# Kernel optimization log

Hardware: AMD Instinct MI355X
Metric: run time of the kernel (lower is better)

## Reference

```python
import jax, jax.numpy as jnp
import numpy as np

B, N, E, H = 2, 50000, 400000, 128


def _lin_init(k, fan_in, fan_out):
    s = 1.0 / np.sqrt(fan_in)
    kw, kb = jax.random.split(k)
    W = jax.random.uniform(kw, (fan_in, fan_out), jnp.float32, -s, s)
    b = jax.random.uniform(kb, (fan_out,), jnp.float32, -s, s)
    return W, b


def setup_inputs() -> dict:
    key = jax.random.key(0)
    ks = jax.random.split(key, 7)
    x = jax.random.normal(ks[0], (B, N, H), jnp.float32)
    edge_index = jax.random.randint(ks[1], (2, E), 0, N, jnp.int64)
    edge_attr = jax.random.normal(ks[2], (B, E, H), jnp.float32)
    We1, be1 = _lin_init(ks[3], 3 * H, H)
    We2, be2 = _lin_init(ks[4], H, H)
    Wn1, bn1 = _lin_init(ks[5], 2 * H, H)
    Wn2, bn2 = _lin_init(ks[6], H, H)
    return dict(x=x, edge_index=edge_index, edge_attr=edge_attr,
                We1=We1, be1=be1, We2=We2, be2=be2,
                Wn1=Wn1, bn1=bn1, Wn2=Wn2, bn2=bn2)


def reference(x, edge_index, edge_attr, We1, be1, We2, be2, Wn1, bn1, Wn2, bn2):
    src = edge_index[0]
    dest = edge_index[1]
    # edge model: MLP(concat(src_feat, dest_feat, edge_attr))  [B,E,3H] -> [B,E,H]
    m = jnp.concatenate([x[:, src], x[:, dest], edge_attr], axis=-1)
    e = jax.nn.relu(m @ We1 + be1) @ We2 + be2
    # node model: scatter-sum messages to dest nodes, then MLP(concat(x, agg))
    agg = jax.vmap(lambda eb: jax.ops.segment_sum(eb, dest, num_segments=x.shape[1]))(e)
    h = jnp.concatenate([x, agg], axis=-1)  # [B,N,2H]
    x_out = jax.nn.relu(h @ Wn1 + bn1) @ Wn2 + bn2
    return x_out, e
```

## Files before the change

kernel.cpp:

```cpp
#include <hip/hip_runtime.h>
#include <hip/hip_bf16.h>

#define Hd 128
#define Nn 50000
#define Ee 400000
#define Bb 2
#define NROWS 100000

typedef __attribute__((ext_vector_type(8))) short bf16x8;
typedef __attribute__((ext_vector_type(4))) short bf16x4;
typedef __attribute__((ext_vector_type(4))) float f32x4;

static __device__ __forceinline__ short f2bf(float f) {
    __hip_bfloat16 h = __float2bfloat16(f);
    return *reinterpret_cast<short*>(&h);
}
static __device__ __forceinline__ float bf2f(short s) {
    union { unsigned u; float f; } v; v.u = ((unsigned)(unsigned short)s) << 16;
    return v.f;
}
static __device__ __forceinline__ bf16x8 cvt8(float4 a, float4 b) {
    bf16x8 r;
    r[0] = f2bf(a.x); r[1] = f2bf(a.y); r[2] = f2bf(a.z); r[3] = f2bf(a.w);
    r[4] = f2bf(b.x); r[5] = f2bf(b.y); r[6] = f2bf(b.z); r[7] = f2bf(b.w);
    return r;
}
static __device__ __forceinline__ unsigned pk2(float a, float b) {
    return (unsigned)(unsigned short)f2bf(a) | ((unsigned)(unsigned short)f2bf(b) << 16);
}

__global__ void prep_weights(const float* __restrict__ We1, const float* __restrict__ We2,
                             const float* __restrict__ Wn1, const float* __restrict__ Wn2,
                             short* __restrict__ wbuf) {
    int gid = blockIdx.x * 256 + threadIdx.x;
    if (gid < 32768) {
        int c = gid >> 7, k = gid & 127;
        float v = (c < 128) ? We1[k * 128 + c] : We1[(k + 128) * 128 + (c - 128)];
        wbuf[gid] = f2bf(v); return;
    }
    int g = gid - 32768;
    if (g < 16384) { int c = g >> 7, k = g & 127; wbuf[gid] = f2bf(We1[(k + 256) * 128 + c]); return; }
    g -= 16384;
    if (g < 16384) { int c = g >> 7, k = g & 127; wbuf[gid] = f2bf(We2[k * 128 + c]); return; }
    g -= 16384;
    if (g < 32768) { int c = g >> 8, k = g & 255; wbuf[gid] = f2bf(Wn1[k * 128 + c]); return; }
    g -= 32768;
    if (g < 16384) { int c = g >> 7, k = g & 127; wbuf[gid] = f2bf(Wn2[k * 128 + c]); }
}

__global__ void hist_kernel(const int* __restrict__ ei, int* __restrict__ cnt) {
    int t = blockIdx.x * 256 + threadIdx.x;
    if (t < Ee) atomicAdd(&cnt[ei[Ee + t]], 1);
}
__global__ void scan1(const int* __restrict__ cnt, int* __restrict__ cur, int* __restrict__ part) {
    __shared__ int s[256];
    int i = blockIdx.x * 256 + threadIdx.x;
    int v = (i < Nn) ? cnt[i] : 0;
    s[threadIdx.x] = v; __syncthreads();
    #pragma unroll
    for (int off = 1; off < 256; off <<= 1) {
        int u = (threadIdx.x >= off) ? s[threadIdx.x - off] : 0;
        __syncthreads(); s[threadIdx.x] += u; __syncthreads();
    }
    if (i < Nn) cur[i] = s[threadIdx.x] - v;
    if (threadIdx.x == 255) part[blockIdx.x] = s[255];
}
__global__ void scan2(int* __restrict__ part) {
    if (threadIdx.x == 0 && blockIdx.x == 0) {
        int run = 0;
        for (int i = 0; i < 196; i++) { int t = part[i]; part[i] = run; run += t; }
    }
}
__global__ void scan3(int* __restrict__ cur, const int* __restrict__ part, int* __restrict__ rp) {
    int i = blockIdx.x * 256 + threadIdx.x;
    if (i < Nn) { int v = cur[i] + part[blockIdx.x]; cur[i] = v; rp[i] = v; }
    if (i == 0 && blockIdx.x == 0) rp[Nn] = Ee;
}
__global__ void scatter_k(const int* __restrict__ ei, int* __restrict__ cur, int* __restrict__ elist) {
    int t = blockIdx.x * 256 + threadIdx.x;
    if (t < Ee) { int d = ei[Ee + t]; int pos = atomicAdd(&cur[d], 1); elist[pos] = t; }
}

__global__ __launch_bounds__(256) void node_pre(
    const float* __restrict__ x, const short* __restrict__ WabT,
    short* __restrict__ xa, short* __restrict__ xb)
{
    __shared__ __align__(16) short X[32 * 128];

    const int nbase = blockIdx.x * 32;
    const int t = threadIdx.x;
    const int wv = t >> 6, lane = t & 63;
    const int row16 = lane & 15, kg = lane >> 4;

    {
        int g = t >> 3, q = t & 7;
        const float* src = x + ((size_t)(nbase + g)) * Hd + q * 16;
        float4 a0 = ((const float4*)src)[0], a1 = ((const float4*)src)[1];
        float4 a2 = ((const float4*)src)[2], a3 = ((const float4*)src)[3];
        ((bf16x8*)X)[g * 16 + ((q * 2) ^ (g & 7))]     = cvt8(a0, a1);
        ((bf16x8*)X)[g * 16 + ((q * 2 + 1) ^ (g & 7))] = cvt8(a2, a3);
    }

    bf16x8 wf[4][4];
    #pragma unroll
    for (int nt = 0; nt < 4; nt++) {
        int n = wv * 64 + nt * 16 + row16;
        #pragma unroll
        for (int kt = 0; kt < 4; kt++)
            wf[kt][nt] = *(const bf16x8*)(WabT + n * 128 + kt * 32 + kg * 8);
    }
    __syncthreads();

    f32x4 acc[2][4];
    #pragma unroll
    for (int mt = 0; mt < 2; mt++)
        #pragma unroll
        for (int nt = 0; nt < 4; nt++) acc[mt][nt] = (f32x4){0.f,0.f,0.f,0.f};

    #pragma unroll
    for (int mt = 0; mt < 2; mt++) {
        int row = mt * 16 + row16;
        #pragma unroll
        for (int kt = 0; kt < 4; kt++) {
            bf16x8 xf = ((const bf16x8*)X)[row * 16 + ((kt * 4 + kg) ^ (row & 7))];
            #pragma unroll
            for (int nt = 0; nt < 4; nt++)
                acc[mt][nt] = __builtin_amdgcn_mfma_f32_16x16x32_bf16(wf[kt][nt], xf, acc[mt][nt], 0, 0, 0);
        }
    }

    #pragma unroll
    for (int mt = 0; mt < 2; mt++) {
        size_t node = nbase + mt * 16 + row16;
        #pragma unroll
        for (int nt = 0; nt < 4; nt++) {
            int ch = wv * 64 + nt * 16 + kg * 4;
            uint2 pk = { pk2(acc[mt][nt][0], acc[mt][nt][1]), pk2(acc[mt][nt][2], acc[mt][nt][3]) };
            short* dst = (ch < 128) ? (xa + node * Hd + ch) : (xb + node * Hd + (ch - 128));
            *(uint2*)dst = pk;
        }
    }
}

__global__ __launch_bounds__(512, 4) void edge_mlp(
    const float* __restrict__ ea, const int* __restrict__ ei,
    const short* __restrict__ xa, const short* __restrict__ xb,
    const short* __restrict__ W1cT, const float* __restrict__ be1,
    const short* __restrict__ W2T, const float* __restrict__ be2,
    float* __restrict__ e_out)
{
    __shared__ __align__(16) short Aea[64 * 128];
    __shared__ __align__(16) short A2[64 * 128];

    const int bid = blockIdx.x;
    const int b = bid / (Ee / 64);
    const int ebase = (bid % (Ee / 64)) * 64;
    const int t = threadIdx.x;
    const int wv = t >> 6, lane = t & 63;
    const int row16 = lane & 15, kg = lane >> 4;
    const int n0 = wv * 16 + kg * 4;

    {
        int row = t >> 3, q = t & 7;
        const float* src = ea + ((size_t)b * Ee + ebase + row) * Hd + q * 16;
        float4 a0 = ((const float4*)src)[0], a1 = ((const float4*)src)[1];
        float4 a2 = ((const float4*)src)[2], a3 = ((const float4*)src)[3];
        ((bf16x8*)Aea)[row * 16 + ((q * 2) ^ (row & 7))]     = cvt8(a0, a1);
        ((bf16x8*)Aea)[row * 16 + ((q * 2 + 1) ^ (row & 7))] = cvt8(a2, a3);
    }

    bf16x8 w1[4];
    {
        const short* wp = W1cT + (wv * 16 + row16) * 128 + kg * 8;
        #pragma unroll
        for (int kt = 0; kt < 4; kt++) w1[kt] = *(const bf16x8*)(wp + kt * 32);
    }
    int sn[4], dn[4];
    #pragma unroll
    for (int mt = 0; mt < 4; mt++) {
        int eidx = ebase + mt * 16 + row16;
        sn[mt] = ei[eidx]; dn[mt] = ei[Ee + eidx];
    }
    __syncthreads();

    f32x4 acc[4];
    #pragma unroll
    for (int mt = 0; mt < 4; mt++) acc[mt] = (f32x4){0.f,0.f,0.f,0.f};
    #pragma unroll
    for (int kt = 0; kt < 4; kt++) {
        #pragma unroll
        for (int mt = 0; mt < 4; mt++) {
            int row = mt * 16 + row16;
            bf16x8 af = ((const bf16x8*)Aea)[row * 16 + ((kt * 4 + kg) ^ (row & 7))];
            acc[mt] = __builtin_amdgcn_mfma_f32_16x16x32_bf16(w1[kt], af, acc[mt], 0, 0, 0);
        }
    }

    bf16x4 av[4], bv[4];
    #pragma unroll
    for (int mt = 0; mt < 4; mt++) {
        av[mt] = *(const bf16x4*)(xa + ((size_t)b * Nn + sn[mt]) * Hd + n0);
        bv[mt] = *(const bf16x4*)(xb + ((size_t)b * Nn + dn[mt]) * Hd + n0);
    }
    float4 b1v = *(const float4*)(be1 + n0);

    bf16x8 w2[4];
    {
        const short* wp = W2T + (wv * 16 + row16) * 128 + kg * 8;
        #pragma unroll
        for (int kt = 0; kt < 4; kt++) w2[kt] = *(const bf16x8*)(wp + kt * 32);
    }

    #pragma unroll
    for (int mt = 0; mt < 4; mt++) {
        int row = mt * 16 + row16;
        float v[4];
        #pragma unroll
        for (int r = 0; r < 4; r++) {
            float u = acc[mt][r] + b1v[r] + bf2f(av[mt][r]) + bf2f(bv[mt][r]);
            v[r] = u > 0.f ? u : 0.f;
        }
        int G = (n0 >> 3) ^ (row & 7);
        *(uint2*)((char*)A2 + row * 256 + G * 16 + (n0 & 7) * 2) = (uint2){ pk2(v[0], v[1]), pk2(v[2], v[3]) };
    }
    __syncthreads();

    f32x4 acc2[4];
    #pragma unroll
    for (int mt = 0; mt < 4; mt++) acc2[mt] = (f32x4){0.f,0.f,0.f,0.f};
    #pragma unroll
    for (int kt = 0; kt < 4; kt++) {
        #pragma unroll
        for (int mt = 0; mt < 4; mt++) {
            int row = mt * 16 + row16;
            bf16x8 hf = *(const bf16x8*)((const char*)A2 + row * 256 + (((kt * 4 + kg) ^ (row & 7)) * 16));
            acc2[mt] = __builtin_amdgcn_mfma_f32_16x16x32_bf16(w2[kt], hf, acc2[mt], 0, 0, 0);
        }
    }
    float4 b2v = *(const float4*)(be2 + n0);
    float* eo = e_out + ((size_t)b * Ee + ebase) * Hd;
    #pragma unroll
    for (int mt = 0; mt < 4; mt++) {
        float4 ov;
        ov.x = acc2[mt][0] + b2v.x;
        ov.y = acc2[mt][1] + b2v.y;
        ov.z = acc2[mt][2] + b2v.z;
        ov.w = acc2[mt][3] + b2v.w;
        *(float4*)(eo + (size_t)(mt * 16 + row16) * Hd + n0) = ov;
    }
}

__global__ __launch_bounds__(512, 4) void node_mlp(
    const float* __restrict__ x, const float* __restrict__ e_out,
    const int* __restrict__ rp, const int* __restrict__ elist,
    const short* __restrict__ Wn1T, const float* __restrict__ bn1,
    const short* __restrict__ Wn2T, const float* __restrict__ bn2,
    float* __restrict__ xout)
{
    __shared__ __align__(16) short A[32 * 256];
    __shared__ __align__(16) short A2[32 * 128];

    const int tilesPerB = (Nn + 31) / 32;
    const int bid = blockIdx.x;
    const int b = bid / tilesPerB;
    const int nbase = (bid % tilesPerB) * 32;
    const int t = threadIdx.x;
    const int wv = t >> 6, lane = t & 63;
    const int row16 = lane & 15, kg = lane >> 4;
    const int n0 = wv * 16 + kg * 4;

    {
        int g = t >> 4, q2 = t & 15;
        int n = nbase + g;
        float4 xv0 = {0,0,0,0}, xv1 = xv0;
        float4 s0 = {0,0,0,0}, s1 = s0;
        if (n < Nn) {
            const float* xr = x + ((size_t)b * Nn + n) * Hd + q2 * 8;
            xv0 = ((const float4*)xr)[0]; xv1 = ((const float4*)xr)[1];
            int jb = rp[n], je = rp[n + 1];
            const float* eb = e_out + (size_t)b * Ee * Hd + q2 * 8;
            int j = jb;
            for (; j + 4 <= je; j += 4) {
                int e0 = elist[j], e1 = elist[j+1], e2 = elist[j+2], e3 = elist[j+3];
                const float* p0 = eb + (size_t)e0 * Hd;
                const float* p1 = eb + (size_t)e1 * Hd;
                const float* p2 = eb + (size_t)e2 * Hd;
                const float* p3 = eb + (size_t)e3 * Hd;
                float4 u0 = ((const float4*)p0)[0], u1 = ((const float4*)p0)[1];
                float4 u2 = ((const float4*)p1)[0], u3 = ((const float4*)p1)[1];
                float4 u4 = ((const float4*)p2)[0], u5 = ((const float4*)p2)[1];
                float4 u6 = ((const float4*)p3)[0], u7 = ((const float4*)p3)[1];
                s0.x += (u0.x + u2.x) + (u4.x + u6.x);
                s0.y += (u0.y + u2.y) + (u4.y + u6.y);
                s0.z += (u0.z + u2.z) + (u4.z + u6.z);
                s0.w += (u0.w + u2.w) + (u4.w + u6.w);
                s1.x += (u1.x + u3.x) + (u5.x + u7.x);
                s1.y += (u1.y + u3.y) + (u5.y + u7.y);
                s1.z += (u1.z + u3.z) + (u5.z + u7.z);
                s1.w += (u1.w + u3.w) + (u5.w + u7.w);
            }
            for (; j < je; j++) {
                const float* p0 = eb + (size_t)elist[j] * Hd;
                float4 u0 = ((const float4*)p0)[0], u1 = ((const float4*)p0)[1];
                s0.x += u0.x; s0.y += u0.y; s0.z += u0.z; s0.w += u0.w;
                s1.x += u1.x; s1.y += u1.y; s1.z += u1.z; s1.w += u1.w;
            }
        }
        ((bf16x8*)A)[g * 32 + (q2 ^ (g & 7))]        = cvt8(xv0, xv1);
        ((bf16x8*)A)[g * 32 + ((16 + q2) ^ (g & 7))] = cvt8(s0, s1);
    }

    bf16x8 w1[8];
    {
        const short* wp = Wn1T + (wv * 16 + row16) * 256 + kg * 8;
        #pragma unroll
        for (int kt = 0; kt < 8; kt++) w1[kt] = *(const bf16x8*)(wp + kt * 32);
    }
    __syncthreads();

    f32x4 acc[2];
    acc[0] = (f32x4){0.f,0.f,0.f,0.f}; acc[1] = (f32x4){0.f,0.f,0.f,0.f};
    #pragma unroll
    for (int kt = 0; kt < 8; kt++) {
        #pragma unroll
        for (int mt = 0; mt < 2; mt++) {
            int row = mt * 16 + row16;
            bf16x8 af = ((const bf16x8*)A)[row * 32 + ((kt * 4 + kg) ^ (row & 7))];
            acc[mt] = __builtin_amdgcn_mfma_f32_16x16x32_bf16(w1[kt], af, acc[mt], 0, 0, 0);
        }
    }

    float4 b1v = *(const float4*)(bn1 + n0);
    bf16x8 w2[4];
    {
        const short* wp = Wn2T + (wv * 16 + row16) * 128 + kg * 8;
        #pragma unroll
        for (int kt = 0; kt < 4; kt++) w2[kt] = *(const bf16x8*)(wp + kt * 32);
    }

    #pragma unroll
    for (int mt = 0; mt < 2; mt++) {
        int row = mt * 16 + row16;
        float v[4];
        #pragma unroll
        for (int r = 0; r < 4; r++) {
            float u = acc[mt][r] + b1v[r];
            v[r] = u > 0.f ? u : 0.f;
        }
        int G = (n0 >> 3) ^ (row & 7);
        *(uint2*)((char*)A2 + row * 256 + G * 16 + (n0 & 7) * 2) = (uint2){ pk2(v[0], v[1]), pk2(v[2], v[3]) };
    }
    __syncthreads();

    f32x4 acc2[2];
    acc2[0] = (f32x4){0.f,0.f,0.f,0.f}; acc2[1] = (f32x4){0.f,0.f,0.f,0.f};
    #pragma unroll
    for (int kt = 0; kt < 4; kt++) {
        #pragma unroll
        for (int mt = 0; mt < 2; mt++) {
            int row = mt * 16 + row16;
            bf16x8 hf = *(const bf16x8*)((const char*)A2 + row * 256 + (((kt * 4 + kg) ^ (row & 7)) * 16));
            acc2[mt] = __builtin_amdgcn_mfma_f32_16x16x32_bf16(w2[kt], hf, acc2[mt], 0, 0, 0);
        }
    }
    float4 b2v = *(const float4*)(bn2 + n0);
    #pragma unroll
    for (int mt = 0; mt < 2; mt++) {
        int node = nbase + mt * 16 + row16;
        if (node < Nn) {
            float4 ov;
            ov.x = acc2[mt][0] + b2v.x;
            ov.y = acc2[mt][1] + b2v.y;
            ov.z = acc2[mt][2] + b2v.z;
            ov.w = acc2[mt][3] + b2v.w;
            *(float4*)(xout + ((size_t)b * Nn + node) * Hd + n0) = ov;
        }
    }
}

extern "C" void kernel_launch(void* const* d_in, const int* in_sizes, int n_in,
                              void* d_out, int out_size, void* d_ws, size_t ws_size,
                              hipStream_t stream) {
    const float* x   = (const float*)d_in[0];
    const int*   ei  = (const int*)d_in[1];
    const float* ea  = (const float*)d_in[2];
    const float* We1 = (const float*)d_in[3];
    const float* be1 = (const float*)d_in[4];
    const float* We2 = (const float*)d_in[5];
    const float* be2 = (const float*)d_in[6];
    const float* Wn1 = (const float*)d_in[7];
    const float* bn1 = (const float*)d_in[8];
    const float* Wn2 = (const float*)d_in[9];
    const float* bn2 = (const float*)d_in[10];

    float* xout  = (float*)d_out;
    float* e_out = xout + (size_t)Bb * Nn * Hd;

    short* wbuf  = (short*)d_ws;
    short* xa    = wbuf + 114688;
    short* xb    = xa + (size_t)NROWS * Hd;
    int*   cnt   = (int*)(xb + (size_t)NROWS * Hd);
    int*   cur   = cnt + Nn;
    int*   rp    = cur + Nn;
    int*   part  = rp + Nn + 1;
    int*   elist = part + 256;

    hipMemsetAsync(cnt, 0, Nn * sizeof(int), stream);
    prep_weights<<<448, 256, 0, stream>>>(We1, We2, Wn1, Wn2, wbuf);
    hist_kernel<<<(Ee + 255) / 256, 256, 0, stream>>>(ei, cnt);
    scan1<<<196, 256, 0, stream>>>(cnt, cur, part);
    scan2<<<1, 64, 0, stream>>>(part);
    scan3<<<196, 256, 0, stream>>>(cur, part, rp);
    scatter_k<<<(Ee + 255) / 256, 256, 0, stream>>>(ei, cur, elist);

    node_pre<<<NROWS / 32, 256, 0, stream>>>(x, wbuf, xa, xb);

    edge_mlp<<<Bb * (Ee / 64), 512, 0, stream>>>(
        ea, ei, xa, xb, wbuf + 32768, be1, wbuf + 49152, be2, e_out);

    node_mlp<<<Bb * ((Nn + 31) / 32), 512, 0, stream>>>(
        x, e_out, rp, elist, wbuf + 65536, bn1, wbuf + 98304, bn2, xout);
}
```

Measured before the change: 505.3 us.

## Make edge MLP persistent over tile chunks with software-pipelined prefetch

Each edge_mlp block now processes a chunk of six 64-edge tiles instead of one, loading the weight fragments once per block. The edge_attr rows, edge indices and gathered node features for the next tile are prefetched into registers while the current tile's MFMAs run, with the LDS staging buffer double-buffered. This aims to hide global-memory latency and amortize weight loads, at the cost of higher register pressure (possibly lower occupancy) and fewer blocks in the grid.

```diff
diff --git a/kernel.cpp b/kernel.cpp
--- a/kernel.cpp
+++ b/kernel.cpp
@@ -6,6 +6,8 @@
 #define Ee 400000
 #define Bb 2
 #define NROWS 100000
+#define NT 12500
+#define CHUNK 6
 
 typedef __attribute__((ext_vector_type(8))) short bf16x8;
 typedef __attribute__((ext_vector_type(4))) short bf16x4;
@@ -27,6 +29,11 @@
 }
 static __device__ __forceinline__ unsigned pk2(float a, float b) {
     return (unsigned)(unsigned short)f2bf(a) | ((unsigned)(unsigned short)f2bf(b) << 16);
+}
+static __device__ __forceinline__ void lds_barrier() {
+    asm volatile("s_waitcnt lgkmcnt(0)" ::: "memory");
+    __builtin_amdgcn_s_barrier();
+    asm volatile("" ::: "memory");
 }
 
 __global__ void prep_weights(const float* __restrict__ We1, const float* __restrict__ We2,
@@ -149,104 +156,157 @@
     const short* __restrict__ W2T, const float* __restrict__ be2,
     float* __restrict__ e_out)
 {
-    __shared__ __align__(16) short Aea[64 * 128];
+    __shared__ __align__(16) short Aea[2][64 * 128];
     __shared__ __align__(16) short A2[64 * 128];
 
-    const int bid = blockIdx.x;
-    const int b = bid / (Ee / 64);
-    const int ebase = (bid % (Ee / 64)) * 64;
     const int t = threadIdx.x;
     const int wv = t >> 6, lane = t & 63;
     const int row16 = lane & 15, kg = lane >> 4;
     const int n0 = wv * 16 + kg * 4;
-
+    const int srow = t >> 3, sq = t & 7;
+
+    bf16x8 w1[4], w2[4];
     {
-        int row = t >> 3, q = t & 7;
-        const float* src = ea + ((size_t)b * Ee + ebase + row) * Hd + q * 16;
-        float4 a0 = ((const float4*)src)[0], a1 = ((const float4*)src)[1];
-        float4 a2 = ((const float4*)src)[2], a3 = ((const float4*)src)[3];
-        ((bf16x8*)Aea)[row * 16 + ((q * 2) ^ (row & 7))]     = cvt8(a0, a1);
-        ((bf16x8*)Aea)[row * 16 + ((q * 2 + 1) ^ (row & 7))] = cvt8(a2, a3);
-    }
-
-    bf16x8 w1[4];
-    {
-        const short* wp = W1cT + (wv * 16 + row16) * 128 + kg * 8;
-        #pragma unroll
-        for (int kt = 0; kt < 4; kt++) w1[kt] = *(const bf16x8*)(wp + kt * 32);
-    }
-    int sn[4], dn[4];
-    #pragma unroll
-    for (int mt = 0; mt < 4; mt++) {
-        int eidx = ebase + mt * 16 + row16;
-        sn[mt] = ei[eidx]; dn[mt] = ei[Ee + eidx];
-    }
-    __syncthreads();
-
-    f32x4 acc[4];
-    #pragma unroll
-    for (int mt = 0; mt < 4; mt++) acc[mt] = (f32x4){0.f,0.f,0.f,0.f};
-    #pragma unroll
-    for (int kt = 0; kt < 4; kt++) {
+        const short* wp1 = W1cT + (wv * 16 + row16) * 128 + kg * 8;
+        const short* wp2 = W2T  + (wv * 16 + row16) * 128 + kg * 8;
+        #pragma unroll
+        for (int kt = 0; kt < 4; kt++) {
+            w1[kt] = *(const bf16x8*)(wp1 + kt * 32);
+            w2[kt] = *(const bf16x8*)(wp2 + kt * 32);
+        }
+    }
+    #pragma unroll
+    for (int kt = 0; kt < 4; kt++) { asm volatile("" : "+v"(w1[kt]), "+v"(w2[kt])); }
+    const float4 b1v = *(const float4*)(be1 + n0);
+    const float4 b2v = *(const float4*)(be2 + n0);
+
+    int tile = blockIdx.x * CHUNK;
+
+    float4 er0, er1, er2, er3;
+    bf16x4 av[4], bv[4];
+    if (tile < NT) {
+        int b = tile / (Ee / 64);
+        int ebase = (tile % (Ee / 64)) * 64;
+        const float* src = ea + ((size_t)b * Ee + ebase + srow) * Hd + sq * 16;
+        er0 = ((const float4*)src)[0]; er1 = ((const float4*)src)[1];
+        er2 = ((const float4*)src)[2]; er3 = ((const float4*)src)[3];
+        int sn[4], dn[4];
         #pragma unroll
         for (int mt = 0; mt < 4; mt++) {
-            int row = mt * 16 + row16;
-            bf16x8 af = ((const bf16x8*)Aea)[row * 16 + ((kt * 4 + kg) ^ (row & 7))];
-            acc[mt] = __builtin_amdgcn_mfma_f32_16x16x32_bf16(w1[kt], af, acc[mt], 0, 0, 0);
-        }
-    }
-
-    bf16x4 av[4], bv[4];
-    #pragma unroll
-    for (int mt = 0; mt < 4; mt++) {
-        av[mt] = *(const bf16x4*)(xa + ((size_t)b * Nn + sn[mt]) * Hd + n0);
-        bv[mt] = *(const bf16x4*)(xb + ((size_t)b * Nn + dn[mt]) * Hd + n0);
-    }
-    float4 b1v = *(const float4*)(be1 + n0);
-
-    bf16x8 w2[4];
-    {
-        const short* wp = W2T + (wv * 16 + row16) * 128 + kg * 8;
-        #pragma unroll
-        for (int kt = 0; kt < 4; kt++) w2[kt] = *(const bf16x8*)(wp + kt * 32);
-    }
-
-    #pragma unroll
-    for (int mt = 0; mt < 4; mt++) {
-        int row = mt * 16 + row16;
-        float v[4];
-        #pragma unroll
-        for (int r = 0; r < 4; r++) {
-            float u = acc[mt][r] + b1v[r] + bf2f(av[mt][r]) + bf2f(bv[mt][r]);
-            v[r] = u > 0.f ? u : 0.f;
-        }
-        int G = (n0 >> 3) ^ (row & 7);
-        *(uint2*)((char*)A2 + row * 256 + G * 16 + (n0 & 7) * 2) = (uint2){ pk2(v[0], v[1]), pk2(v[2], v[3]) };
-    }
-    __syncthreads();
-
-    f32x4 acc2[4];
-    #pragma unroll
-    for (int mt = 0; mt < 4; mt++) acc2[mt] = (f32x4){0.f,0.f,0.f,0.f};
-    #pragma unroll
-    for (int kt = 0; kt < 4; kt++) {
+            int eidx = ebase + mt * 16 + row16;
+            sn[mt] = ei[eidx]; dn[mt] = ei[Ee + eidx];
+        }
+        const short* xab = xa + (size_t)b * Nn * Hd;
+        const short* xbb = xb + (size_t)b * Nn * Hd;
         #pragma unroll
         for (int mt = 0; mt < 4; mt++) {
-            int row = mt * 16 + row16;
-            bf16x8 hf = *(const bf16x8*)((const char*)A2 + row * 256 + (((kt * 4 + kg) ^ (row & 7)) * 16));
-            acc2[mt] = __builtin_amdgcn_mfma_f32_16x16x32_bf16(w2[kt], hf, acc2[mt], 0, 0, 0);
-        }
-    }
-    float4 b2v = *(const float4*)(be2 + n0);
-    float* eo = e_out + ((size_t)b * Ee + ebase) * Hd;
-    #pragma unroll
-    for (int mt = 0; mt < 4; mt++) {
-        float4 ov;
-        ov.x = acc2[mt][0] + b2v.x;
-        ov.y = acc2[mt][1] + b2v.y;
-        ov.z = acc2[mt][2] + b2v.z;
-        ov.w = acc2[mt][3] + b2v.w;
-        *(float4*)(eo + (size_t)(mt * 16 + row16) * Hd + n0) = ov;
+            av[mt] = *(const bf16x4*)(xab + (size_t)sn[mt] * Hd + n0);
+            bv[mt] = *(const bf16x4*)(xbb + (size_t)dn[mt] * Hd + n0);
+        }
+    }
+
+    int cur = 0;
+    for (int it = 0; it < CHUNK; ++it) {
+        const bool v = (tile < NT);
+        const int b = tile / (Ee / 64);
+        const size_t ebase = (size_t)(tile % (Ee / 64)) * 64;
+
+        if (v) {
+            ((bf16x8*)Aea[cur])[srow * 16 + ((sq * 2)     ^ (srow & 7))] = cvt8(er0, er1);
+            ((bf16x8*)Aea[cur])[srow * 16 + ((sq * 2 + 1) ^ (srow & 7))] = cvt8(er2, er3);
+        }
+        lds_barrier();
+
+        const int ntile = tile + 1;
+        const bool nv = (it + 1 < CHUNK) && (ntile < NT);
+        float4 ner0, ner1, ner2, ner3;
+        int nsn[4], ndn[4];
+        int nb = 0; int nebase = 0;
+        if (nv) {
+            nb = ntile / (Ee / 64);
+            nebase = (ntile % (Ee / 64)) * 64;
+            const float* src = ea + ((size_t)nb * Ee + nebase + srow) * Hd + sq * 16;
+            ner0 = ((const float4*)src)[0]; ner1 = ((const float4*)src)[1];
+            ner2 = ((const float4*)src)[2]; ner3 = ((const float4*)src)[3];
+            #pragma unroll
+            for (int mt = 0; mt < 4; mt++) {
+                int eidx = nebase + mt * 16 + row16;
+                nsn[mt] = ei[eidx]; ndn[mt] = ei[Ee + eidx];
+            }
+        }
+
+        f32x4 acc[4];
+        #pragma unroll
+        for (int mt = 0; mt < 4; mt++) acc[mt] = (f32x4){0.f,0.f,0.f,0.f};
+        if (v) {
+            #pragma unroll
+            for (int kt = 0; kt < 4; kt++) {
+                #pragma unroll
+                for (int mt = 0; mt < 4; mt++) {
+                    int row = mt * 16 + row16;
+                    bf16x8 af = ((const bf16x8*)Aea[cur])[row * 16 + ((kt * 4 + kg) ^ (row & 7))];
+                    acc[mt] = __builtin_amdgcn_mfma_f32_16x16x32_bf16(w1[kt], af, acc[mt], 0, 0, 0);
+                }
+            }
+        }
+
+        bf16x4 nav[4], nbv[4];
+        if (nv) {
+            const short* xab = xa + (size_t)nb * Nn * Hd;
+            const short* xbb = xb + (size_t)nb * Nn * Hd;
+            #pragma unroll
+            for (int mt = 0; mt < 4; mt++) {
+                nav[mt] = *(const bf16x4*)(xab + (size_t)nsn[mt] * Hd + n0);
+                nbv[mt] = *(const bf16x4*)(xbb + (size_t)ndn[mt] * Hd + n0);
+            }
+        }
+
+        if (v) {
+            #pragma unroll
+            for (int mt = 0; mt < 4; mt++) {
+                int row = mt * 16 + row16;
+                float vv[4];
+                #pragma unroll
+                for (int r = 0; r < 4; r++) {
+                    float u = acc[mt][r] + b1v[r] + bf2f(av[mt][r]) + bf2f(bv[mt][r]);
+                    vv[r] = u > 0.f ? u : 0.f;
+                }
+                int G = (n0 >> 3) ^ (row & 7);
+                *(uint2*)((char*)A2 + row * 256 + G * 16 + (n0 & 7) * 2) =
+                    (uint2){ pk2(vv[0], vv[1]), pk2(vv[2], vv[3]) };
+            }
+        }
+        lds_barrier();
+
+        if (v) {
+            f32x4 acc2[4];
+            #pragma unroll
+            for (int mt = 0; mt < 4; mt++) acc2[mt] = (f32x4){0.f,0.f,0.f,0.f};
+            #pragma unroll
+            for (int kt = 0; kt < 4; kt++) {
+                #pragma unroll
+                for (int mt = 0; mt < 4; mt++) {
+                    int row = mt * 16 + row16;
+                    bf16x8 hf = *(const bf16x8*)((const char*)A2 + row * 256 + (((kt * 4 + kg) ^ (row & 7)) * 16));
+                    acc2[mt] = __builtin_amdgcn_mfma_f32_16x16x32_bf16(w2[kt], hf, acc2[mt], 0, 0, 0);
+                }
+            }
+            float* eo = e_out + ((size_t)b * Ee + ebase) * Hd;
+            #pragma unroll
+            for (int mt = 0; mt < 4; mt++) {
+                float4 ov;
+                ov.x = acc2[mt][0] + b2v.x;
+                ov.y = acc2[mt][1] + b2v.y;
+                ov.z = acc2[mt][2] + b2v.z;
+                ov.w = acc2[mt][3] + b2v.w;
+                *(float4*)(eo + (size_t)(mt * 16 + row16) * Hd + n0) = ov;
+            }
+        }
+
+        er0 = ner0; er1 = ner1; er2 = ner2; er3 = ner3;
+        #pragma unroll
+        for (int mt = 0; mt < 4; mt++) { av[mt] = nav[mt]; bv[mt] = nbv[mt]; }
+        cur ^= 1; tile = ntile;
     }
 }
 
@@ -415,7 +475,7 @@
 
     node_pre<<<NROWS / 32, 256, 0, stream>>>(x, wbuf, xa, xb);
 
-    edge_mlp<<<Bb * (Ee / 64), 512, 0, stream>>>(
+    edge_mlp<<<(NT + CHUNK - 1) / CHUNK, 512, 0, stream>>>(
         ea, ei, xa, xb, wbuf + 32768, be1, wbuf + 49152, be2, e_out);
 
     node_mlp<<<Bb * ((Nn + 31) / 32), 512, 0, stream>>>(
```

Measured after the change: 580.3 us. 14.8% more time.

## Pre-gather summed src/dest node projections into a contiguous edge buffer

Applied to the files above, without the earlier changes.

Adds an xs_pre kernel that gathers the per-edge src and dest projected node features, adds them, and writes a contiguous bf16 [B,E,H] buffer. The edge MLP kernel then reads this buffer with coalesced loads instead of doing random gathers inside the MFMA kernel. It also replaces the barriers with an explicit lgkmcnt wait plus s_barrier. The cost is an extra kernel launch and about 200 MB of extra write and read traffic. The path is only taken when the workspace is large enough, otherwise the old gather kernel runs.

```diff
diff --git a/kernel.cpp b/kernel.cpp
--- a/kernel.cpp
+++ b/kernel.cpp
@@ -6,6 +6,8 @@
 #define Ee 400000
 #define Bb 2
 #define NROWS 100000
+#define TPB 6250
+#define NT 12500
 
 typedef __attribute__((ext_vector_type(8))) short bf16x8;
 typedef __attribute__((ext_vector_type(4))) short bf16x4;
@@ -27,6 +29,10 @@
 }
 static __device__ __forceinline__ unsigned pk2(float a, float b) {
     return (unsigned)(unsigned short)f2bf(a) | ((unsigned)(unsigned short)f2bf(b) << 16);
+}
+static __device__ __forceinline__ void lds_barrier() {
+    asm volatile("s_waitcnt lgkmcnt(0)" ::: "memory");
+    __builtin_amdgcn_s_barrier();
 }
 
 __global__ void prep_weights(const float* __restrict__ We1, const float* __restrict__ We2,
@@ -142,7 +148,129 @@
     }
 }
 
-__global__ __launch_bounds__(512, 4) void edge_mlp(
+__global__ __launch_bounds__(256) void xs_pre(
+    const int* __restrict__ ei, const short* __restrict__ xa,
+    const short* __restrict__ xb, short* __restrict__ xs)
+{
+    int gid = blockIdx.x * 256 + threadIdx.x;
+    int c = gid & 3;
+    int e = (gid >> 2) % Ee;
+    int b = gid / (Ee * 4);
+    int s = ei[e], d = ei[Ee + e];
+    const short* xar = xa + ((size_t)b * Nn + s) * Hd + c * 32;
+    const short* xbr = xb + ((size_t)b * Nn + d) * Hd + c * 32;
+    short* dst = xs + ((size_t)b * Ee + e) * Hd + c * 32;
+    #pragma unroll
+    for (int g = 0; g < 4; g++) {
+        bf16x8 a8 = ((const bf16x8*)xar)[g];
+        bf16x8 b8 = ((const bf16x8*)xbr)[g];
+        bf16x8 o;
+        #pragma unroll
+        for (int j = 0; j < 8; j++) o[j] = f2bf(bf2f(a8[j]) + bf2f(b8[j]));
+        ((bf16x8*)dst)[g] = o;
+    }
+}
+
+__global__ __launch_bounds__(512) void edge_mlp_xs(
+    const float* __restrict__ ea, const short* __restrict__ xs,
+    const short* __restrict__ W1cT, const float* __restrict__ be1,
+    const short* __restrict__ W2T, const float* __restrict__ be2,
+    float* __restrict__ e_out)
+{
+    __shared__ __align__(16) short Aea[64 * 128];
+    __shared__ __align__(16) short A2[64 * 128];
+
+    const int bid = blockIdx.x;
+    const int b = bid / TPB;
+    const size_t ebase = (size_t)(bid % TPB) * 64;
+    const int t = threadIdx.x;
+    const int wv = t >> 6, lane = t & 63;
+    const int row16 = lane & 15, kg = lane >> 4;
+    const int n0 = wv * 16 + kg * 4;
+
+    {
+        int row = t >> 3, q = t & 7;
+        const float* src = ea + ((size_t)b * Ee + ebase + row) * Hd + q * 16;
+        float4 a0 = ((const float4*)src)[0], a1 = ((const float4*)src)[1];
+        float4 a2 = ((const float4*)src)[2], a3 = ((const float4*)src)[3];
+        ((bf16x8*)Aea)[row * 16 + ((q * 2) ^ (row & 7))]     = cvt8(a0, a1);
+        ((bf16x8*)Aea)[row * 16 + ((q * 2 + 1) ^ (row & 7))] = cvt8(a2, a3);
+    }
+
+    bf16x8 w1[4], w2[4];
+    {
+        const short* wp1 = W1cT + (wv * 16 + row16) * 128 + kg * 8;
+        const short* wp2 = W2T  + (wv * 16 + row16) * 128 + kg * 8;
+        #pragma unroll
+        for (int kt = 0; kt < 4; kt++) {
+            w1[kt] = *(const bf16x8*)(wp1 + kt * 32);
+            w2[kt] = *(const bf16x8*)(wp2 + kt * 32);
+        }
+    }
+    bf16x4 xv[4];
+    {
+        const short* xsb = xs + ((size_t)b * Ee + ebase) * Hd + n0;
+        #pragma unroll
+        for (int mt = 0; mt < 4; mt++)
+            xv[mt] = *(const bf16x4*)(xsb + (size_t)(mt * 16 + row16) * Hd);
+    }
+    const float4 b1v = *(const float4*)(be1 + n0);
+    const float4 b2v = *(const float4*)(be2 + n0);
+    lds_barrier();
+
+    f32x4 acc[4];
+    #pragma unroll
+    for (int mt = 0; mt < 4; mt++) acc[mt] = (f32x4){0.f,0.f,0.f,0.f};
+    #pragma unroll
+    for (int kt = 0; kt < 4; kt++) {
+        #pragma unroll
+        for (int mt = 0; mt < 4; mt++) {
+            int row = mt * 16 + row16;
+            bf16x8 af = ((const bf16x8*)Aea)[row * 16 + ((kt * 4 + kg) ^ (row & 7))];
+            acc[mt] = __builtin_amdgcn_mfma_f32_16x16x32_bf16(w1[kt], af, acc[mt], 0, 0, 0);
+        }
+    }
+
+    #pragma unroll
+    for (int mt = 0; mt < 4; mt++) {
+        int row = mt * 16 + row16;
+        float vv[4];
+        #pragma unroll
+        for (int r = 0; r < 4; r++) {
+            float u = acc[mt][r] + b1v[r] + bf2f(xv[mt][r]);
+            vv[r] = u > 0.f ? u : 0.f;
+        }
+        int G = (n0 >> 3) ^ (row & 7);
+        *(uint2*)((char*)A2 + row * 256 + G * 16 + (n0 & 7) * 2) =
+            (uint2){ pk2(vv[0], vv[1]), pk2(vv[2], vv[3]) };
+    }
+    lds_barrier();
+
+    f32x4 acc2[4];
+    #pragma unroll
+    for (int mt = 0; mt < 4; mt++) acc2[mt] = (f32x4){0.f,0.f,0.f,0.f};
+    #pragma unroll
+    for (int kt = 0; kt < 4; kt++) {
+        #pragma unroll
+        for (int mt = 0; mt < 4; mt++) {
+            int row = mt * 16 + row16;
+            bf16x8 hf = *(const bf16x8*)((const char*)A2 + row * 256 + (((kt * 4 + kg) ^ (row & 7)) * 16));
+            acc2[mt] = __builtin_amdgcn_mfma_f32_16x16x32_bf16(w2[kt], hf, acc2[mt], 0, 0, 0);
+        }
+    }
+    float* eo = e_out + ((size_t)b * Ee + ebase) * Hd;
+    #pragma unroll
+    for (int mt = 0; mt < 4; mt++) {
+        float4 ov;
+        ov.x = acc2[mt][0] + b2v.x;
+        ov.y = acc2[mt][1] + b2v.y;
+        ov.z = acc2[mt][2] + b2v.z;
+        ov.w = acc2[mt][3] + b2v.w;
+        *(float4*)(eo + (size_t)(mt * 16 + row16) * Hd + n0) = ov;
+    }
+}
+
+__global__ __launch_bounds__(512, 4) void edge_mlp_gather(
     const float* __restrict__ ea, const int* __restrict__ ei,
     const short* __restrict__ xa, const short* __restrict__ xb,
     const short* __restrict__ W1cT, const float* __restrict__ be1,
@@ -153,8 +281,8 @@
     __shared__ __align__(16) short A2[64 * 128];
 
     const int bid = blockIdx.x;
-    const int b = bid / (Ee / 64);
-    const int ebase = (bid % (Ee / 64)) * 64;
+    const int b = bid / TPB;
+    const size_t ebase = (size_t)(bid % TPB) * 64;
     const int t = threadIdx.x;
     const int wv = t >> 6, lane = t & 63;
     const int row16 = lane & 15, kg = lane >> 4;
@@ -168,7 +296,6 @@
         ((bf16x8*)Aea)[row * 16 + ((q * 2) ^ (row & 7))]     = cvt8(a0, a1);
         ((bf16x8*)Aea)[row * 16 + ((q * 2 + 1) ^ (row & 7))] = cvt8(a2, a3);
     }
-
     bf16x8 w1[4];
     {
         const short* wp = W1cT + (wv * 16 + row16) * 128 + kg * 8;
@@ -178,7 +305,7 @@
     int sn[4], dn[4];
     #pragma unroll
     for (int mt = 0; mt < 4; mt++) {
-        int eidx = ebase + mt * 16 + row16;
+        int eidx = (int)ebase + mt * 16 + row16;
         sn[mt] = ei[eidx]; dn[mt] = ei[Ee + eidx];
     }
     __syncthreads();
@@ -195,7 +322,6 @@
             acc[mt] = __builtin_amdgcn_mfma_f32_16x16x32_bf16(w1[kt], af, acc[mt], 0, 0, 0);
         }
     }
-
     bf16x4 av[4], bv[4];
     #pragma unroll
     for (int mt = 0; mt < 4; mt++) {
@@ -203,14 +329,12 @@
         bv[mt] = *(const bf16x4*)(xb + ((size_t)b * Nn + dn[mt]) * Hd + n0);
     }
     float4 b1v = *(const float4*)(be1 + n0);
-
     bf16x8 w2[4];
     {
         const short* wp = W2T + (wv * 16 + row16) * 128 + kg * 8;
         #pragma unroll
         for (int kt = 0; kt < 4; kt++) w2[kt] = *(const bf16x8*)(wp + kt * 32);
     }
-
     #pragma unroll
     for (int mt = 0; mt < 4; mt++) {
         int row = mt * 16 + row16;
@@ -396,14 +520,18 @@
     float* xout  = (float*)d_out;
     float* e_out = xout + (size_t)Bb * Nn * Hd;
 
-    short* wbuf  = (short*)d_ws;
-    short* xa    = wbuf + 114688;
+    char* w = (char*)d_ws;
+    short* wbuf  = (short*)w;
+    short* xa    = (short*)(w + 229376);
     short* xb    = xa + (size_t)NROWS * Hd;
     int*   cnt   = (int*)(xb + (size_t)NROWS * Hd);
     int*   cur   = cnt + Nn;
     int*   rp    = cur + Nn;
     int*   part  = rp + Nn + 1;
     int*   elist = part + 256;
+    short* xs    = (short*)(elist + Ee);
+    size_t need  = (size_t)((char*)(xs + (size_t)Bb * Ee * Hd) - w);
+    bool use_xs  = (ws_size >= need);
 
     hipMemsetAsync(cnt, 0, Nn * sizeof(int), stream);
     prep_weights<<<448, 256, 0, stream>>>(We1, We2, Wn1, Wn2, wbuf);
@@ -415,8 +543,14 @@
 
     node_pre<<<NROWS / 32, 256, 0, stream>>>(x, wbuf, xa, xb);
 
-    edge_mlp<<<Bb * (Ee / 64), 512, 0, stream>>>(
-        ea, ei, xa, xb, wbuf + 32768, be1, wbuf + 49152, be2, e_out);
+    if (use_xs) {
+        xs_pre<<<(Bb * Ee * 4) / 256, 256, 0, stream>>>(ei, xa, xb, xs);
+        edge_mlp_xs<<<NT, 512, 0, stream>>>(
+            ea, xs, wbuf + 32768, be1, wbuf + 49152, be2, e_out);
+    } else {
+        edge_mlp_gather<<<NT, 512, 0, stream>>>(
+            ea, ei, xa, xb, wbuf + 32768, be1, wbuf + 49152, be2, e_out);
+    }
 
     node_mlp<<<Bb * ((Nn + 31) / 32), 512, 0, stream>>>(
         x, e_out, rp, elist, wbuf + 65536, bn1, wbuf + 98304, bn2, xout);
```

Measured after the change: 563.8 us. +11.6%, slower.

## Fuse scatter-sum into edge MLP via dest-sorted edge tiles and atomics

Applied to the files above, without the earlier changes.

The edge MLP now processes edges in destination-sorted order through elist. It segment-reduces each 16-row group in LDS and atomically adds the partial sums into a zeroed fp32 agg buffer. The node MLP then reads agg directly instead of gathering e_out rows through a CSR pointer array. This removes the second full read of the large edge output, at the cost of gathered edge_attr reads, scattered e_out writes, atomics and an extra memset of agg. Barriers are also replaced with lighter LDS-only barriers, and weight and feature loads are hoisted.

```diff
diff --git a/kernel.cpp b/kernel.cpp
--- a/kernel.cpp
+++ b/kernel.cpp
@@ -6,6 +6,8 @@
 #define Ee 400000
 #define Bb 2
 #define NROWS 100000
+#define TPB 6250
+#define NT 12500
 
 typedef __attribute__((ext_vector_type(8))) short bf16x8;
 typedef __attribute__((ext_vector_type(4))) short bf16x4;
@@ -27,6 +29,10 @@
 }
 static __device__ __forceinline__ unsigned pk2(float a, float b) {
     return (unsigned)(unsigned short)f2bf(a) | ((unsigned)(unsigned short)f2bf(b) << 16);
+}
+static __device__ __forceinline__ void lds_barrier() {
+    asm volatile("s_waitcnt lgkmcnt(0)" ::: "memory");
+    __builtin_amdgcn_s_barrier();
 }
 
 __global__ void prep_weights(const float* __restrict__ We1, const float* __restrict__ We2,
@@ -71,10 +77,9 @@
         for (int i = 0; i < 196; i++) { int t = part[i]; part[i] = run; run += t; }
     }
 }
-__global__ void scan3(int* __restrict__ cur, const int* __restrict__ part, int* __restrict__ rp) {
+__global__ void scan3(int* __restrict__ cur, const int* __restrict__ part) {
     int i = blockIdx.x * 256 + threadIdx.x;
-    if (i < Nn) { int v = cur[i] + part[blockIdx.x]; cur[i] = v; rp[i] = v; }
-    if (i == 0 && blockIdx.x == 0) rp[Nn] = Ee;
+    if (i < Nn) cur[i] += part[blockIdx.x];
 }
 __global__ void scatter_k(const int* __restrict__ ei, int* __restrict__ cur, int* __restrict__ elist) {
     int t = blockIdx.x * 256 + threadIdx.x;
@@ -142,46 +147,70 @@
     }
 }
 
-__global__ __launch_bounds__(512, 4) void edge_mlp(
+__global__ __launch_bounds__(512) void edge_mlp(
     const float* __restrict__ ea, const int* __restrict__ ei,
+    const int* __restrict__ elist,
     const short* __restrict__ xa, const short* __restrict__ xb,
     const short* __restrict__ W1cT, const float* __restrict__ be1,
     const short* __restrict__ W2T, const float* __restrict__ be2,
-    float* __restrict__ e_out)
+    float* __restrict__ e_out, float* __restrict__ agg)
 {
-    __shared__ __align__(16) short Aea[64 * 128];
-    __shared__ __align__(16) short A2[64 * 128];
-
-    const int bid = blockIdx.x;
-    const int b = bid / (Ee / 64);
-    const int ebase = (bid % (Ee / 64)) * 64;
+    __shared__ __align__(16) char smem[32768 + 768];
+    short* Aea = (short*)smem;
+    short* A2  = (short*)(smem + 16384);
+    int* ol = (int*)(smem + 32768);
+    int* sl = ol + 64;
+    int* dl = sl + 64;
+
+    const int tile = blockIdx.x;
+    const int b = tile / TPB;
+    const int w0 = (tile % TPB) * 64;
     const int t = threadIdx.x;
     const int wv = t >> 6, lane = t & 63;
     const int row16 = lane & 15, kg = lane >> 4;
     const int n0 = wv * 16 + kg * 4;
-
-    {
-        int row = t >> 3, q = t & 7;
-        const float* src = ea + ((size_t)b * Ee + ebase + row) * Hd + q * 16;
+    const int srow = t >> 3, sq = t & 7;
+
+    if (t < 64) {
+        int o = elist[w0 + t];
+        ol[t] = o; sl[t] = ei[o]; dl[t] = ei[Ee + o];
+    }
+    __syncthreads();
+
+    int on[4], sn[4], dn[4];
+    #pragma unroll
+    for (int mt = 0; mt < 4; mt++) {
+        int r = mt * 16 + row16;
+        on[mt] = ol[r]; sn[mt] = sl[r]; dn[mt] = dl[r];
+    }
+
+    {
+        const float* src = ea + ((size_t)b * Ee + ol[srow]) * Hd + sq * 16;
         float4 a0 = ((const float4*)src)[0], a1 = ((const float4*)src)[1];
         float4 a2 = ((const float4*)src)[2], a3 = ((const float4*)src)[3];
-        ((bf16x8*)Aea)[row * 16 + ((q * 2) ^ (row & 7))]     = cvt8(a0, a1);
-        ((bf16x8*)Aea)[row * 16 + ((q * 2 + 1) ^ (row & 7))] = cvt8(a2, a3);
-    }
-
-    bf16x8 w1[4];
-    {
-        const short* wp = W1cT + (wv * 16 + row16) * 128 + kg * 8;
-        #pragma unroll
-        for (int kt = 0; kt < 4; kt++) w1[kt] = *(const bf16x8*)(wp + kt * 32);
-    }
-    int sn[4], dn[4];
+        ((bf16x8*)Aea)[srow * 16 + ((sq * 2) ^ (srow & 7))]     = cvt8(a0, a1);
+        ((bf16x8*)Aea)[srow * 16 + ((sq * 2 + 1) ^ (srow & 7))] = cvt8(a2, a3);
+    }
+
+    bf16x8 w1[4], w2[4];
+    {
+        const short* wp1 = W1cT + (wv * 16 + row16) * 128 + kg * 8;
+        const short* wp2 = W2T  + (wv * 16 + row16) * 128 + kg * 8;
+        #pragma unroll
+        for (int kt = 0; kt < 4; kt++) {
+            w1[kt] = *(const bf16x8*)(wp1 + kt * 32);
+            w2[kt] = *(const bf16x8*)(wp2 + kt * 32);
+        }
+    }
+    bf16x4 av[4], bv[4];
     #pragma unroll
     for (int mt = 0; mt < 4; mt++) {
-        int eidx = ebase + mt * 16 + row16;
-        sn[mt] = ei[eidx]; dn[mt] = ei[Ee + eidx];
-    }
-    __syncthreads();
+        av[mt] = *(const bf16x4*)(xa + ((size_t)b * Nn + sn[mt]) * Hd + n0);
+        bv[mt] = *(const bf16x4*)(xb + ((size_t)b * Nn + dn[mt]) * Hd + n0);
+    }
+    const float4 b1v = *(const float4*)(be1 + n0);
+    const float4 b2v = *(const float4*)(be2 + n0);
+    lds_barrier();
 
     f32x4 acc[4];
     #pragma unroll
@@ -196,34 +225,20 @@
         }
     }
 
-    bf16x4 av[4], bv[4];
-    #pragma unroll
-    for (int mt = 0; mt < 4; mt++) {
-        av[mt] = *(const bf16x4*)(xa + ((size_t)b * Nn + sn[mt]) * Hd + n0);
-        bv[mt] = *(const bf16x4*)(xb + ((size_t)b * Nn + dn[mt]) * Hd + n0);
-    }
-    float4 b1v = *(const float4*)(be1 + n0);
-
-    bf16x8 w2[4];
-    {
-        const short* wp = W2T + (wv * 16 + row16) * 128 + kg * 8;
-        #pragma unroll
-        for (int kt = 0; kt < 4; kt++) w2[kt] = *(const bf16x8*)(wp + kt * 32);
-    }
-
     #pragma unroll
     for (int mt = 0; mt < 4; mt++) {
         int row = mt * 16 + row16;
-        float v[4];
+        float vv[4];
         #pragma unroll
         for (int r = 0; r < 4; r++) {
             float u = acc[mt][r] + b1v[r] + bf2f(av[mt][r]) + bf2f(bv[mt][r]);
-            v[r] = u > 0.f ? u : 0.f;
+            vv[r] = u > 0.f ? u : 0.f;
         }
         int G = (n0 >> 3) ^ (row & 7);
-        *(uint2*)((char*)A2 + row * 256 + G * 16 + (n0 & 7) * 2) = (uint2){ pk2(v[0], v[1]), pk2(v[2], v[3]) };
-    }
-    __syncthreads();
+        *(uint2*)((char*)A2 + row * 256 + G * 16 + (n0 & 7) * 2) =
+            (uint2){ pk2(vv[0], vv[1]), pk2(vv[2], vv[3]) };
+    }
+    lds_barrier();
 
     f32x4 acc2[4];
     #pragma unroll
@@ -237,22 +252,47 @@
             acc2[mt] = __builtin_amdgcn_mfma_f32_16x16x32_bf16(w2[kt], hf, acc2[mt], 0, 0, 0);
         }
     }
-    float4 b2v = *(const float4*)(be2 + n0);
-    float* eo = e_out + ((size_t)b * Ee + ebase) * Hd;
+
+    float ev[4][4];
     #pragma unroll
     for (int mt = 0; mt < 4; mt++) {
-        float4 ov;
-        ov.x = acc2[mt][0] + b2v.x;
-        ov.y = acc2[mt][1] + b2v.y;
-        ov.z = acc2[mt][2] + b2v.z;
-        ov.w = acc2[mt][3] + b2v.w;
-        *(float4*)(eo + (size_t)(mt * 16 + row16) * Hd + n0) = ov;
+        #pragma unroll
+        for (int r = 0; r < 4; r++) ev[mt][r] = acc2[mt][r] + b1v[r] * 0.f + ((const float*)&b2v)[r];
+        float4 ov = { ev[mt][0], ev[mt][1], ev[mt][2], ev[mt][3] };
+        *(float4*)(e_out + ((size_t)b * Ee + on[mt]) * Hd + n0) = ov;
+    }
+    lds_barrier();
+
+    #pragma unroll
+    for (int mt = 0; mt < 4; mt++) {
+        int row = mt * 16 + row16;
+        float4 ov = { ev[mt][0], ev[mt][1], ev[mt][2], ev[mt][3] };
+        *(float4*)(smem + row * 512 + (((n0 >> 2) ^ (row & 7)) << 4)) = ov;
+    }
+    lds_barrier();
+
+    {
+        int c = t & 127, rg = t >> 7;
+        int g_c = c >> 2, sub = (c & 3) << 2;
+        float s = 0.f;
+        int pd = dl[rg * 16];
+        #pragma unroll
+        for (int i = 0; i < 16; i++) {
+            int row = rg * 16 + i;
+            float v = *(const float*)(smem + row * 512 + ((g_c ^ (row & 7)) << 4) + sub);
+            int d = dl[row];
+            if (d != pd) {
+                unsafeAtomicAdd(agg + ((size_t)b * Nn + pd) * Hd + c, s);
+                s = 0.f; pd = d;
+            }
+            s += v;
+        }
+        unsafeAtomicAdd(agg + ((size_t)b * Nn + pd) * Hd + c, s);
     }
 }
 
 __global__ __launch_bounds__(512, 4) void node_mlp(
-    const float* __restrict__ x, const float* __restrict__ e_out,
-    const int* __restrict__ rp, const int* __restrict__ elist,
+    const float* __restrict__ x, const float* __restrict__ agg,
     const short* __restrict__ Wn1T, const float* __restrict__ bn1,
     const short* __restrict__ Wn2T, const float* __restrict__ bn2,
     float* __restrict__ xout)
@@ -277,34 +317,8 @@
         if (n < Nn) {
             const float* xr = x + ((size_t)b * Nn + n) * Hd + q2 * 8;
             xv0 = ((const float4*)xr)[0]; xv1 = ((const float4*)xr)[1];
-            int jb = rp[n], je = rp[n + 1];
-            const float* eb = e_out + (size_t)b * Ee * Hd + q2 * 8;
-            int j = jb;
-            for (; j + 4 <= je; j += 4) {
-                int e0 = elist[j], e1 = elist[j+1], e2 = elist[j+2], e3 = elist[j+3];
-                const float* p0 = eb + (size_t)e0 * Hd;
-                const float* p1 = eb + (size_t)e1 * Hd;
-                const float* p2 = eb + (size_t)e2 * Hd;
-                const float* p3 = eb + (size_t)e3 * Hd;
-                float4 u0 = ((const float4*)p0)[0], u1 = ((const float4*)p0)[1];
-                float4 u2 = ((const float4*)p1)[0], u3 = ((const float4*)p1)[1];
-                float4 u4 = ((const float4*)p2)[0], u5 = ((const float4*)p2)[1];
-                float4 u6 = ((const float4*)p3)[0], u7 = ((const float4*)p3)[1];
-                s0.x += (u0.x + u2.x) + (u4.x + u6.x);
-                s0.y += (u0.y + u2.y) + (u4.y + u6.y);
-                s0.z += (u0.z + u2.z) + (u4.z + u6.z);
-                s0.w += (u0.w + u2.w) + (u4.w + u6.w);
-                s1.x += (u1.x + u3.x) + (u5.x + u7.x);
-                s1.y += (u1.y + u3.y) + (u5.y + u7.y);
-                s1.z += (u1.z + u3.z) + (u5.z + u7.z);
-                s1.w += (u1.w + u3.w) + (u5.w + u7.w);
-            }
-            for (; j < je; j++) {
-                const float* p0 = eb + (size_t)elist[j] * Hd;
-                float4 u0 = ((const float4*)p0)[0], u1 = ((const float4*)p0)[1];
-                s0.x += u0.x; s0.y += u0.y; s0.z += u0.z; s0.w += u0.w;
-                s1.x += u1.x; s1.y += u1.y; s1.z += u1.z; s1.w += u1.w;
-            }
+            const float* ar = agg + ((size_t)b * Nn + n) * Hd + q2 * 8;
+            s0 = ((const float4*)ar)[0]; s1 = ((const float4*)ar)[1];
         }
         ((bf16x8*)A)[g * 32 + (q2 ^ (g & 7))]        = cvt8(xv0, xv1);
         ((bf16x8*)A)[g * 32 + ((16 + q2) ^ (g & 7))] = cvt8(s0, s1);
@@ -396,28 +410,31 @@
     float* xout  = (float*)d_out;
     float* e_out = xout + (size_t)Bb * Nn * Hd;
 
-    short* wbuf  = (short*)d_ws;
-    short* xa    = wbuf + 114688;
+    char* w = (char*)d_ws;
+    short* wbuf  = (short*)w;
+    short* xa    = (short*)(w + 229376);
     short* xb    = xa + (size_t)NROWS * Hd;
-    int*   cnt   = (int*)(xb + (size_t)NROWS * Hd);
+    float* agg   = (float*)(xb + (size_t)NROWS * Hd);
+    int*   cnt   = (int*)(agg + (size_t)Bb * Nn * Hd);
     int*   cur   = cnt + Nn;
-    int*   rp    = cur + Nn;
-    int*   part  = rp + Nn + 1;
+    int*   part  = cur + Nn;
     int*   elist = part + 256;
 
     hipMemsetAsync(cnt, 0, Nn * sizeof(int), stream);
+    hipMemsetAsync(agg, 0, (size_t)Bb * Nn * Hd * sizeof(float), stream);
+
     prep_weights<<<448, 256, 0, stream>>>(We1, We2, Wn1, Wn2, wbuf);
     hist_kernel<<<(Ee + 255) / 256, 256, 0, stream>>>(ei, cnt);
     scan1<<<196, 256, 0, stream>>>(cnt, cur, part);
     scan2<<<1, 64, 0, stream>>>(part);
-    scan3<<<196, 256, 0, stream>>>(cur, part, rp);
+    scan3<<<196, 256, 0, stream>>>(cur, part);
     scatter_k<<<(Ee + 255) / 256, 256, 0, stream>>>(ei, cur, elist);
 
     node_pre<<<NROWS / 32, 256, 0, stream>>>(x, wbuf, xa, xb);
 
-    edge_mlp<<<Bb * (Ee / 64), 512, 0, stream>>>(
-        ea, ei, xa, xb, wbuf + 32768, be1, wbuf + 49152, be2, e_out);
+    edge_mlp<<<NT, 512, 0, stream>>>(
+        ea, ei, elist, xa, xb, wbuf + 32768, be1, wbuf + 49152, be2, e_out, agg);
 
     node_mlp<<<Bb * ((Nn + 31) / 32), 512, 0, stream>>>(
-        x, e_out, rp, elist, wbuf + 65536, bn1, wbuf + 98304, bn2, xout);
-}
+        x, agg, wbuf + 65536, bn1, wbuf + 98304, bn2, xout);
+}
```

New measurement: 496.7 us. No clear change (-1.7%).
